# Kernel optimization log

Hardware: AMD Instinct MI355X
Metric: run time of the kernel (lower is better)

## Reference

```python
import jax, jax.numpy as jnp
import numpy as np

B, T, F, H, O = 256, 1024, 128, 512, 64
BN_EPS = 1e-5


def setup_inputs() -> dict:
    key = jax.random.key(0)
    ks = jax.random.split(key, 24)
    p = lambda k, shape: 0.02 * jax.random.normal(k, shape, dtype=jnp.float32)
    inp = {
        "x": jax.random.normal(ks[0], (B, T, F), dtype=jnp.float32),
        "delta": jax.random.uniform(ks[1], (B, T, F), dtype=jnp.float32),
        "m": (jax.random.uniform(ks[2], (B, T, F)) > 0.5).astype(jnp.float32),
        "x_forward": jax.random.normal(ks[3], (B, T, F), dtype=jnp.float32),
        # packed-sequence style: descending number of active rows per timestep
        "batch_sizes": jnp.sort(jax.random.randint(ks[4], (T,), 1, B + 1))[::-1].astype(jnp.int32),
        "W_r": p(ks[5], (F, H)), "U_r": p(ks[6], (H, H)), "V_r": p(ks[7], (F, H)), "b_r": jnp.zeros((H,), jnp.float32),
        "W_z": p(ks[8], (F, H)), "U_z": p(ks[9], (H, H)), "V_z": p(ks[10], (F, H)), "b_z": jnp.zeros((H,), jnp.float32),
        "W": p(ks[11], (F, H)), "U": p(ks[12], (H, H)), "V": p(ks[13], (F, H)), "b": jnp.zeros((H,), jnp.float32),
        "W_gamma_x": p(ks[14], (F,)), "b_gamma_x": jnp.zeros((F,), jnp.float32),
        "W_gamma_h": p(ks[15], (F, H)), "b_gamma_h": jnp.zeros((H,), jnp.float32),
        "dec_W": p(ks[16], (H, O)), "dec_b": jnp.zeros((O,), jnp.float32),
        "bn_w": jnp.ones((H,), jnp.float32), "bn_b": jnp.zeros((H,), jnp.float32),
    }
    return inp


def reference(x, delta, m, x_forward, batch_sizes,
              W_r, U_r, V_r, b_r, W_z, U_z, V_z, b_z, W, U, V, b,
              W_gamma_x, b_gamma_x, W_gamma_h, b_gamma_h,
              dec_W, dec_b, bn_w, bn_b):
    # input decay gamma_x: [B,T,F]; hidden decay gamma_h: [B,T,H]
    gamma_x = jnp.exp(-jax.nn.relu(delta * W_gamma_x + b_gamma_x))
    gamma_h = jnp.exp(-jax.nn.relu(jnp.einsum("btf,fh->bth", m, W_gamma_h) + b_gamma_h))
    # impute observed (m==1) positions with decayed forward-fill (matches x[m.byte()] = x_replace[m.byte()])
    x_rep = gamma_x * x_forward + (1.0 - gamma_x) * 0.001
    x = jnp.where(m > 0.5, x_rep, x)

    # time-major for scan
    xT = jnp.transpose(x, (1, 0, 2))        # [T,B,F]
    mT = jnp.transpose(m, (1, 0, 2))        # [T,B,F]
    gT = jnp.transpose(gamma_h, (1, 0, 2))  # [T,B,H]
    row = jnp.arange(B)

    def step(h, inp):
        x_t, m_t, g_t, bs = inp
        mask = (row < bs)[:, None]          # active rows this step
        h_d = jnp.where(mask, g_t * h, h)   # decayed hidden (index_copy_ on [:bs])
        one_m = 1.0 - m_t
        z = jax.nn.sigmoid(x_t @ W_z + h_d @ U_z + one_m @ V_z + b_z)
        r = jax.nn.sigmoid(x_t @ W_r + h_d @ U_r + one_m @ V_r + b_r)
        h_tilde = jnp.tanh(x_t @ W + (h_d * r) @ U + one_m @ V + b)
        h_new = jnp.where(mask, (1.0 - z) * h_d + z * h_tilde, h_d)
        return h_new, None

    h0 = jnp.zeros((B, H), jnp.float32)
    h_t, _ = jax.lax.scan(step, h0, (xT, mT, gT, batch_sizes))

    # eval-mode BatchNorm1d (running_mean=0, running_var=1); batch_size>1 so BN applies
    h_bn = h_t * (bn_w / jnp.sqrt(1.0 + BN_EPS)) + bn_b
    output = jax.nn.log_softmax(h_bn @ dec_W + dec_b, axis=-1)
    return output, h_bn
```

## Files before the change

kernel.cpp:

```cpp
#include <hip/hip_runtime.h>
#include <hip/hip_bf16.h>

typedef __attribute__((ext_vector_type(8))) short bf16x8;
typedef __attribute__((ext_vector_type(4))) float f32x4;
typedef __attribute__((ext_vector_type(4))) float fvec4;
typedef __attribute__((ext_vector_type(4))) unsigned short u16x4;
typedef __attribute__((ext_vector_type(4))) int i32x4;
typedef __attribute__((ext_vector_type(2))) unsigned int u32x2;

#define DEVI __device__ __forceinline__

constexpr int BB = 256, TT = 1024, FF = 128, HH = 512, OO = 64;
constexpr int KK = 256;
constexpr int NN = 2048;

DEVI unsigned short f2bf(float x) {
  unsigned int u = __float_as_uint(x);
  u += 0x7FFFu + ((u >> 16) & 1u);
  return (unsigned short)(u >> 16);
}
DEVI float bf2f(unsigned short s) {
  return __uint_as_float(((unsigned int)s) << 16);
}

DEVI void gload16(const void* g, void* lds) {
  __builtin_amdgcn_global_load_lds(
      (const __attribute__((address_space(1))) void*)g,
      (__attribute__((address_space(3))) void*)lds, 16, 0, 0);
}

DEVI void barrier_lds() {
  asm volatile("s_waitcnt lgkmcnt(0)" ::: "memory");
  __builtin_amdgcn_s_barrier();
  __builtin_amdgcn_sched_barrier(0);
}

DEVI int hgIdx(int row, int c) { return row*1024 + (c ^ ((row & 7) << 3)); }

__global__ __launch_bounds__(256) void prep_scales_kernel(
    const float* __restrict__ U_z, const float* __restrict__ U_r,
    const float* __restrict__ Uh, float* __restrict__ uscale)
{
  int n = blockIdx.x * 256 + threadIdx.x;
  if (n >= 1536) return;
  const float* src = (n < 512) ? U_z : (n < 1024) ? U_r : Uh;
  int col = n & 511;
  float s = 0.f;
  for (int k = 0; k < HH; ++k) s = fmaxf(s, fabsf(src[k*HH + col]));
  uscale[n] = fmaxf(s, 1e-30f);
}

__global__ __launch_bounds__(256) void prep_kernel(
    const float* __restrict__ W_z, const float* __restrict__ V_z, const float* __restrict__ b_z,
    const float* __restrict__ W_r, const float* __restrict__ V_r, const float* __restrict__ b_r,
    const float* __restrict__ Wh,  const float* __restrict__ Vh,  const float* __restrict__ bh,
    const float* __restrict__ Wgh, const float* __restrict__ bgh,
    const float* __restrict__ U_z, const float* __restrict__ U_r, const float* __restrict__ Uh,
    const float* __restrict__ uscale,
    unsigned short* __restrict__ BwT, float* __restrict__ bias,
    unsigned int* __restrict__ UzrN, int* __restrict__ UhQ)
{
  int idx = blockIdx.x * 256 + threadIdx.x;
  if (idx < 524288) {
    int n = idx >> 8, k = idx & 255;
    float v;
    if (n < 512)       { int h = n;        v = (k < 128) ? W_z[k*HH + h] : -V_z[(k-128)*HH + h]; }
    else if (n < 1024) { int h = n - 512;  v = (k < 128) ? W_r[k*HH + h] : -V_r[(k-128)*HH + h]; }
    else if (n < 1536) { int h = n - 1024; v = (k < 128) ? Wh [k*HH + h] : -Vh [(k-128)*HH + h]; }
    else               { int h = n - 1536; v = (k < 128) ? 0.f : Wgh[(k-128)*HH + h]; }
    BwT[n*256 + k] = f2bf(v);
    return;
  }
  idx -= 524288;
  if (idx < 2048) {
    int n = idx; float v;
    if (n < 512)       { float s = b_z[n];      for (int f = 0; f < FF; ++f) s += V_z[f*HH + n];        v = s; }
    else if (n < 1024) { int h = n-512;  float s = b_r[h]; for (int f = 0; f < FF; ++f) s += V_r[f*HH + h]; v = s; }
    else if (n < 1536) { int h = n-1024; float s = bh[h];  for (int f = 0; f < FF; ++f) s += Vh[f*HH + h];  v = s; }
    else               { v = bgh[n-1536]; }
    bias[n] = v;
    return;
  }
  idx -= 2048;
  if (idx < 65536) {
    int c  = idx & 1;
    int l  = (idx >> 1) & 63;
    int i  = (idx >> 7) & 3;
    int wv = (idx >> 9) & 7;
    int u  = idx >> 12;
    int kt = u >> 1, half = u & 1;
    int col = (wv*4 + i)*16 + (l & 15);
    const float* src = half ? U_r : U_z;
    float sc = 7.f / uscale[half*512 + col];
    unsigned int word = 0;
#pragma unroll
    for (int p = 0; p < 8; ++p) {
      int j = c*8 + (p & 1)*4 + (p >> 1);
      int k = kt*64 + (l >> 4)*16 + j;
      float q = fminf(fmaxf(rintf(src[k*HH + col] * sc), -7.f), 7.f);
      unsigned int uq = (unsigned int)((int)q + 8);
      word |= (uq & 0xF) << (4*p);
    }
    UzrN[idx] = word;
    return;
  }
  idx -= 65536;
  if (idx < 65536) {
    int j0 = (idx & 3) * 4;
    int l  = (idx >> 2) & 63;
    int nt = (idx >> 8) & 31;
    int kt = idx >> 13;
    int col = nt*16 + (l & 15);
    float sc = 127.f / uscale[1024 + col];
    int word = 0;
#pragma unroll
    for (int b = 0; b < 4; ++b) {
      int k = kt*64 + (l >> 4)*16 + j0 + b;
      float q = fminf(fmaxf(rintf(Uh[k*HH + col] * sc), -127.f), 127.f);
      word |= ((int)q & 0xFF) << (8*b);
    }
    UhQ[idx] = word;
  }
}

__global__ __launch_bounds__(256) void build_A_kernel(
    const float* __restrict__ x, const float* __restrict__ delta,
    const float* __restrict__ mm, const float* __restrict__ xf,
    const float* __restrict__ Wgx, const float* __restrict__ bgx,
    const int* __restrict__ bs, unsigned short* __restrict__ A,
    int t0, int TC)
{
  int blk = blockIdx.x;
  int row8 = blk * 8;
  int b0  = row8 / TC;
  int tl0 = row8 % TC;
  if (b0 >= bs[t0 + tl0]) return;
  int tid = threadIdx.x;
  int rl = row8 + (tid >> 5);
  int tc = tl0 + (tid >> 5);
  long gi = ((long)b0*TT + t0 + tc) * 32 + (tid & 31);
  int f0 = (tid & 31) * 4;
  fvec4 xv = ((const fvec4*)x)[gi];
  fvec4 dv = ((const fvec4*)delta)[gi];
  fvec4 mv = ((const fvec4*)mm)[gi];
  fvec4 fv = ((const fvec4*)xf)[gi];
  unsigned short ox[4], om[4];
#pragma unroll
  for (int j = 0; j < 4; ++j) {
    float g  = __expf(-fmaxf(dv[j]*Wgx[f0+j] + bgx[f0+j], 0.f));
    float xr = g*fv[j] + (1.f - g)*0.001f;
    float xi = (mv[j] > 0.5f) ? xr : xv[j];
    ox[j] = f2bf(xi); om[j] = f2bf(mv[j]);
  }
  *(u16x4*)(A + (long)rl*KK + f0)       = (u16x4){ox[0], ox[1], ox[2], ox[3]};
  *(u16x4*)(A + (long)rl*KK + 128 + f0) = (u16x4){om[0], om[1], om[2], om[3]};
}

__global__ __launch_bounds__(256) void gemm1_kernel(
    const unsigned short* __restrict__ A, const unsigned short* __restrict__ BwT,
    const float* __restrict__ bias, const int* __restrict__ bs,
    unsigned short* __restrict__ PRE, int t0, int TC)
{
  int blk = blockIdx.x;
  int nt = blk & 15;
  int mt = blk >> 4;
  {
    int m0 = mt * 128;
    int b_ = m0 / TC;
    int bcheck = (TC >= 128) ? bs[t0 + (m0 % TC)] : bs[t0];
    if (b_ >= bcheck) return;
  }
  int tid = threadIdx.x;
  int w = tid >> 6, l = tid & 63;
  int wm = w >> 1, wn = w & 1;
  int lr = l & 15, lg = l >> 4;
  int m_base = mt*128 + wm*64;
  int n_base = nt*128 + wn*64;
  const unsigned short* Aptr = A   + (long)(m_base + lr)*KK + lg*8;
  const unsigned short* Bptr = BwT + (long)(n_base + lr)*KK + lg*8;
  f32x4 acc[4][4];
#pragma unroll
  for (int i = 0; i < 4; ++i)
#pragma unroll
    for (int j = 0; j < 4; ++j) acc[i][j] = (f32x4){0.f, 0.f, 0.f, 0.f};

#pragma unroll
  for (int kt = 0; kt < 8; ++kt) {
    bf16x8 af[4], bfr[4];
#pragma unroll
    for (int i = 0; i < 4; ++i) af[i]  = *(const bf16x8*)(Aptr + (long)i*16*KK + kt*32);
#pragma unroll
    for (int i = 0; i < 4; ++i) bfr[i] = *(const bf16x8*)(Bptr + (long)i*16*KK + kt*32);
#pragma unroll
    for (int ms = 0; ms < 4; ++ms)
#pragma unroll
      for (int ns = 0; ns < 4; ++ns)
        acc[ms][ns] = __builtin_amdgcn_mfma_f32_16x16x32_bf16(af[ms], bfr[ns], acc[ms][ns], 0, 0, 0);
  }
#pragma unroll
  for (int ms = 0; ms < 4; ++ms) {
    int gm0 = m_base + ms*16 + lg*4;
#pragma unroll
    for (int ns = 0; ns < 4; ++ns) {
      int gn = n_base + ns*16 + lr;
      float bv = bias[gn];
      bool is_gamma = (gn >= 1536);
#pragma unroll
      for (int q = 0; q < 4; ++q) {
        float v = acc[ms][ns][q] + bv;
        if (is_gamma) v = __expf(-fmaxf(v, 0.f));
        PRE[(long)(gm0 + q)*NN + gn] = f2bf(v);
      }
    }
  }
}

__global__ __launch_bounds__(512, 2) void scan_kernel(
    const unsigned short* __restrict__ PRE,
    const unsigned int* __restrict__ UzrN,
    const signed char* __restrict__ UhQ,
    const float* __restrict__ uscale,
    const int* __restrict__ bs,
    float* __restrict__ h_st,
    float* __restrict__ sbuf,
    int t0, int TC)
{
  __shared__ __align__(16) signed char Ubuf[8][2][4096];
  __shared__ __align__(16) i32x4 hd_l[8*64];
  __shared__ __align__(16) unsigned short slabHG[16*1024];
  __shared__ float hm[16][524];
  __shared__ int hsumW[8][16];
  __shared__ float wmax[8];

  const int tid = threadIdx.x;
  const int r0 = blockIdx.x * 16;
  if (t0 > 0 && bs[t0] <= r0) return;

  const int w = tid >> 6, l = tid & 63, lr = l & 15, lg = l >> 4;
  const size_t rowStr = (size_t)TC * NN;

  signed char* slot0 = &Ubuf[w][0][0];
  signed char* slot1 = &Ubuf[w][1][0];

  auto STAGEB = [&](int u) {
    const signed char* src = UhQ + ((size_t)((u*32 + w*4)*64) + l)*16;
    signed char* dst = (u & 1) ? slot1 : slot0;
#pragma unroll
    for (int i = 0; i < 4; ++i) gload16(src + (size_t)i*1024, dst + i*1024);
  };
  auto STAGEHG = [&](const unsigned short* PREn) {
#pragma unroll
    for (int j = 0; j < 4; ++j) {
      int idx = w*4 + j;
      int row = idx >> 1;
      int phys = (idx & 1)*512 + l*8;
      int logi = phys ^ ((row & 7) << 3);
      const unsigned short* src = PREn + (size_t)row*rowStr + 1024 + logi;
      gload16(src, &slabHG[idx*512]);
    }
  };
  auto LOADZR = [&](int u, u32x2* d) {
#pragma unroll
    for (int i = 0; i < 4; ++i)
      d[i] = ((const u32x2*)UzrN)[((u*8 + w)*4 + i)*64 + l];
  };

  float zdq[4], rdq[4], hdq[4];
#pragma unroll
  for (int i = 0; i < 4; ++i) {
    int c = (w*4 + i)*16 + lr;
    zdq[i] = uscale[c]        * (1.f/889.f);
    rdq[i] = uscale[512 + c]  * (1.f/889.f);
    hdq[i] = uscale[1024 + c] * (1.f/16129.f);
  }
  if (tid < 8) wmax[tid] = (t0 == 0) ? 1e-20f : sbuf[blockIdx.x];

  if (t0 == 0) {
    for (int i = tid; i < 16*512; i += 512) hm[i>>9][i&511] = 0.f;
  } else {
    for (int i = tid; i < 16*512; i += 512)
      hm[i>>9][i&511] = h_st[(size_t)(r0 + (i>>9))*HH + (i&511)];
  }
  asm volatile("s_waitcnt vmcnt(0)" ::: "memory");
  __builtin_amdgcn_sched_barrier(0);

  STAGEHG(PRE + (size_t)r0*TC*NN);
  STAGEB(0); STAGEB(1);

  for (int tc = 0; tc < TC; ++tc) {
    const int bsv = bs[t0 + tc];
    if (bsv <= r0) break;
    const int na = min(16, bsv - r0);
    const unsigned short* PREstep = PRE + ((size_t)r0*TC + tc)*NN;
    const unsigned short* PREnext = PREstep + NN;

    barrier_lds();
    asm volatile("s_waitcnt vmcnt(8)" ::: "memory");
    __builtin_amdgcn_sched_barrier(0);

    float s = wmax[0];
#pragma unroll
    for (int i = 1; i < 8; ++i) s = fmaxf(s, wmax[i]);
    const float qs = 127.f / s;

    unsigned short pzr[2][4][4];
#pragma unroll
    for (int i = 0; i < 4; ++i)
#pragma unroll
      for (int q = 0; q < 4; ++q) {
        int row = lg*4 + q, col = (w*4 + i)*16 + lr;
        const unsigned short* pb = PREstep + (size_t)row*rowStr + col;
        pzr[0][i][q] = pb[0];
        pzr[1][i][q] = pb[512];
      }

    u32x2 inW0[4], inW1[4];
    LOADZR(0, inW0);
    LOADZR(1, inW1);

    {
      const int k0 = w*64 + lg*16;
      const bool act = lr < na;
      bf16x8 g0 = *(const bf16x8*)&slabHG[hgIdx(lr, 512 + k0)];
      bf16x8 g1 = *(const bf16x8*)&slabHG[hgIdx(lr, 512 + k0 + 8)];
      i32x4 qw;
      int psum = 0;
#pragma unroll
      for (int d = 0; d < 4; ++d) {
        int word = 0;
#pragma unroll
        for (int b = 0; b < 4; ++b) {
          int j = d*4 + b;
          float h  = hm[lr][k0 + j];
          float gv = bf2f((unsigned short)(j < 8 ? g0[j] : g1[j-8]));
          float hd = act ? gv*h : h;
          float q  = fminf(fmaxf(rintf(hd*qs), -127.f), 127.f);
          int qi = (int)q;
          psum += qi;
          word |= (qi & 0xFF) << (8*b);
        }
        qw[d] = word;
      }
      hd_l[w*64 + l] = qw;
      psum += __shfl_xor(psum, 16);
      psum += __shfl_xor(psum, 32);
      if (lg == 0) hsumW[w][lr] = psum;
    }

    float phv[4][4], ggv[4][4];
#pragma unroll
    for (int i = 0; i < 4; ++i)
#pragma unroll
      for (int q = 0; q < 4; ++q) {
        int row = lg*4 + q, col = (w*4 + i)*16 + lr;
        phv[i][q] = bf2f(slabHG[hgIdx(row, col)]);
        ggv[i][q] = bf2f(slabHG[hgIdx(row, 512 + col)]);
      }
    barrier_lds();

    i32x4 acc[8];
#pragma unroll
    for (int i = 0; i < 8; ++i) acc[i] = (i32x4){0, 0, 0, 0};
    i32x4 af;
#pragma unroll
    for (int u = 0; u < 16; ++u) {
      if (!(u & 1)) af = hd_l[(u>>1)*64 + l];
      u32x2* inw = (u & 1) ? inW1 : inW0;
      __builtin_amdgcn_s_setprio(1);
#pragma unroll
      for (int i = 0; i < 4; ++i) {
        unsigned int W0 = inw[i][0], W1 = inw[i][1];
        i32x4 bfr;
        bfr[0] = (int)(W0 & 0x0F0F0F0Fu);
        bfr[1] = (int)((W0 >> 4) & 0x0F0F0F0Fu);
        bfr[2] = (int)(W1 & 0x0F0F0F0Fu);
        bfr[3] = (int)((W1 >> 4) & 0x0F0F0F0Fu);
        acc[(u&1)*4 + i] = __builtin_amdgcn_mfma_i32_16x16x64_i8(af, bfr, acc[(u&1)*4 + i], 0, 0, 0);
      }
      __builtin_amdgcn_s_setprio(0);
      if (u < 14) LOADZR(u + 2, (u & 1) ? inW1 : inW0);
    }

    int rsum[4];
#pragma unroll
    for (int q = 0; q < 4; ++q) {
      int row = lg*4 + q, t = 0;
#pragma unroll
      for (int w2 = 0; w2 < 8; ++w2) t += hsumW[w2][row];
      rsum[q] = t * 8;
    }
    float zreg[4][4];
#pragma unroll
    for (int i = 0; i < 4; ++i)
#pragma unroll
      for (int q = 0; q < 4; ++q) {
        int row = lg*4 + q, col = (w*4 + i)*16 + lr;
        float az = bf2f(pzr[0][i][q]) + (float)(acc[i][q]   - rsum[q]) * zdq[i] * s;
        float ar = bf2f(pzr[1][i][q]) + (float)(acc[4+i][q] - rsum[q]) * rdq[i] * s;
        zreg[i][q] = 1.f/(1.f + __expf(-az));
        slabHG[hgIdx(row, col)] = f2bf(1.f/(1.f + __expf(-ar)));
      }
    barrier_lds();

    {
      const int k0 = w*64 + lg*16;
      bf16x8 r0v = *(const bf16x8*)&slabHG[hgIdx(lr, k0)];
      bf16x8 r1v = *(const bf16x8*)&slabHG[hgIdx(lr, k0 + 8)];
      i32x4 qw = hd_l[w*64 + l], nw;
#pragma unroll
      for (int d = 0; d < 4; ++d) {
        int word = qw[d], out = 0;
#pragma unroll
        for (int b = 0; b < 4; ++b) {
          int j = d*4 + b;
          int hq = (int)(signed char)((word >> (8*b)) & 0xFF);
          float rv = bf2f((unsigned short)(j < 8 ? r0v[j] : r1v[j-8]));
          float q = fminf(fmaxf(rintf((float)hq * rv), -127.f), 127.f);
          out |= ((int)q & 0xFF) << (8*b);
        }
        nw[d] = out;
      }
      hd_l[w*64 + l] = nw;
    }
    barrier_lds();

    i32x4 accB[4];
#pragma unroll
    for (int i = 0; i < 4; ++i) accB[i] = (i32x4){0, 0, 0, 0};
#pragma unroll
    for (int u = 0; u < 8; ++u) {
      asm volatile("s_waitcnt vmcnt(4)" ::: "memory");
      __builtin_amdgcn_sched_barrier(0);
      const signed char* buf = (u & 1) ? slot1 : slot0;
      i32x4 af2 = hd_l[u*64 + l];
      __builtin_amdgcn_s_setprio(1);
#pragma unroll
      for (int i = 0; i < 4; ++i) {
        i32x4 bfr = ((const i32x4*)buf)[i*64 + l];
        accB[i] = __builtin_amdgcn_mfma_i32_16x16x64_i8(af2, bfr, accB[i], 0, 0, 0);
      }
      __builtin_amdgcn_s_setprio(0);
      __builtin_amdgcn_sched_barrier(0);
      if (u < 6)       STAGEB(u + 2);
      else if (u == 6) STAGEHG(PREnext);
      else             STAGEB(0);
    }
    STAGEB(1);

    float mloc = 0.f;
#pragma unroll
    for (int i = 0; i < 4; ++i)
#pragma unroll
      for (int q = 0; q < 4; ++q) {
        int row = lg*4 + q, col = (w*4 + i)*16 + lr;
        float hval;
        if (row < na) {
          float ah = phv[i][q] + (float)accB[i][q] * hdq[i] * s;
          float e  = __expf(2.f*ah);
          float th = 1.f - 2.f/(e + 1.f);
          float hd = ggv[i][q] * hm[row][col];
          hval = hd + zreg[i][q]*(th - hd);
          hm[row][col] = hval;
        } else {
          hval = hm[row][col];
        }
        mloc = fmaxf(mloc, fabsf(hval));
      }
#pragma unroll
    for (int off = 32; off > 0; off >>= 1) mloc = fmaxf(mloc, __shfl_xor(mloc, off));
    if (l == 0) wmax[w] = fmaxf(mloc, 1e-20f);
  }

  asm volatile("s_waitcnt vmcnt(0)" ::: "memory");
  barrier_lds();
  for (int i = tid; i < 16*512; i += 512)
    h_st[(size_t)(r0 + (i>>9))*HH + (i&511)] = hm[i>>9][i&511];
  if (tid == 0) {
    float s = wmax[0];
#pragma unroll
    for (int i = 1; i < 8; ++i) s = fmaxf(s, wmax[i]);
    sbuf[blockIdx.x] = s;
  }
}

__global__ __launch_bounds__(64) void head_kernel(
    const float* __restrict__ h_state, const float* __restrict__ decW,
    const float* __restrict__ decb, const float* __restrict__ bnw,
    const float* __restrict__ bnb, float* __restrict__ out)
{
  int b = blockIdx.x, o = threadIdx.x;
  __shared__ float hbn[HH];
  const float s = rsqrtf(1.f + 1e-5f);
  for (int j = o; j < HH; j += 64)
    hbn[j] = h_state[(long)b*HH + j] * (bnw[j] * s) + bnb[j];
  __syncthreads();
  float acc = decb[o];
  for (int j = 0; j < HH; ++j) acc += hbn[j] * decW[j*OO + o];
  float mx = acc;
#pragma unroll
  for (int off = 32; off > 0; off >>= 1) mx = fmaxf(mx, __shfl_xor(mx, off));
  float ex = __expf(acc - mx);
  float sum = ex;
#pragma unroll
  for (int off = 32; off > 0; off >>= 1) sum += __shfl_xor(sum, off);
  out[(long)b*OO + o] = acc - mx - __logf(sum);
  for (int j = o; j < HH; j += 64)
    out[(long)BB*OO + (long)b*HH + j] = hbn[j];
}

extern "C" void kernel_launch(void* const* d_in, const int* in_sizes, int n_in,
                              void* d_out, int out_size, void* d_ws, size_t ws_size,
                              hipStream_t stream) {
  const float* x     = (const float*)d_in[0];
  const float* delta = (const float*)d_in[1];
  const float* mm    = (const float*)d_in[2];
  const float* xf    = (const float*)d_in[3];
  const int*   bs    = (const int*)  d_in[4];
  const float* W_r   = (const float*)d_in[5];
  const float* U_r   = (const float*)d_in[6];
  const float* V_r   = (const float*)d_in[7];
  const float* b_r   = (const float*)d_in[8];
  const float* W_z   = (const float*)d_in[9];
  const float* U_z   = (const float*)d_in[10];
  const float* V_z   = (const float*)d_in[11];
  const float* b_z   = (const float*)d_in[12];
  const float* W     = (const float*)d_in[13];
  const float* U     = (const float*)d_in[14];
  const float* V     = (const float*)d_in[15];
  const float* b     = (const float*)d_in[16];
  const float* Wgx   = (const float*)d_in[17];
  const float* bgx   = (const float*)d_in[18];
  const float* Wgh   = (const float*)d_in[19];
  const float* bgh   = (const float*)d_in[20];
  const float* decW  = (const float*)d_in[21];
  const float* decb  = (const float*)d_in[22];
  const float* bnw   = (const float*)d_in[23];
  const float* bnb   = (const float*)d_in[24];

  auto rnd = [](size_t v) { return (v + 255) & ~(size_t)255; };
  const size_t fixed_bytes = rnd((size_t)2048*256*2) + rnd(2048*4)
                           + rnd((size_t)256*1024) + rnd((size_t)256*1024)
                           + rnd(1536*4) + rnd(64)
                           + rnd((size_t)BB*HH*4);
  int TC = 0;
  const int cands[5] = {128, 64, 32, 16, 8};
  for (int i = 0; i < 5; ++i) {
    size_t need = fixed_bytes + rnd((size_t)BB*cands[i]*KK*2) + rnd((size_t)BB*cands[i]*NN*2);
    if (need <= ws_size) { TC = cands[i]; break; }
  }
  if (TC == 0) return;

  char* p = (char*)d_ws;
  auto alloc = [&](size_t bytes) { char* r = p; p += (bytes + 255) & ~(size_t)255; return r; };
  unsigned short* A_chunk = (unsigned short*)alloc((size_t)BB * TC * KK * 2);
  unsigned short* PREc    = (unsigned short*)alloc((size_t)BB * TC * NN * 2);
  unsigned short* BwT     = (unsigned short*)alloc((size_t)2048 * 256 * 2);
  float*          bias    = (float*)alloc(2048 * 4);
  unsigned int*   UzrN    = (unsigned int*)alloc((size_t)256 * 1024);
  int*            UhQ     = (int*)alloc((size_t)256 * 1024);
  float*          uscale  = (float*)alloc(1536 * 4);
  float*          sbuf    = (float*)alloc(64);
  float*          h_st    = (float*)alloc((size_t)BB * HH * 4);

  prep_scales_kernel<<<6, 256, 0, stream>>>(U_z, U_r, U, uscale);
  prep_kernel<<<2568, 256, 0, stream>>>(W_z, V_z, b_z, W_r, V_r, b_r, W, V, b,
                                        Wgh, bgh, U_z, U_r, U, uscale,
                                        BwT, bias, UzrN, UhQ);
  const int nch = TT / TC;
  for (int c = 0; c < nch; ++c) {
    int t0 = c * TC;
    build_A_kernel<<<BB*TC/8, 256, 0, stream>>>(x, delta, mm, xf, Wgx, bgx, bs,
                                                A_chunk, t0, TC);
    gemm1_kernel<<<(BB*TC/128)*16, 256, 0, stream>>>(A_chunk, BwT, bias, bs,
                                                     PREc, t0, TC);
    scan_kernel<<<16, 512, 0, stream>>>(PREc, UzrN, (const signed char*)UhQ,
                                        uscale, bs, h_st, sbuf, t0, TC);
  }
  head_kernel<<<256, 64, 0, stream>>>(h_st, decW, decb, bnw, bnb, (float*)d_out);
}
```

Baseline: 20.83 ms.

## Quantize U_h recurrent weights to int4 and deepen the staging pipeline

The candidate-state recurrent weight U_h is now stored as offset-4-bit nibbles instead of int8, which halves its bytes streamed per timestep. The nibbles are unpacked to int8 with masks before the i8 MFMA, and the +8 offset is removed with a per-row sum of the activations. The LDS staging for U_h grows from two to four slots, and the U_z/U_r register prefetch grows to four stages, with the wait counts adjusted to match. The trade is a coarser quantization of U_h, which costs accuracy, plus extra unpack ALU work and more registers.

```diff
diff --git a/kernel.cpp b/kernel.cpp
--- a/kernel.cpp
+++ b/kernel.cpp
@@ -58,7 +58,7 @@
     const float* __restrict__ U_z, const float* __restrict__ U_r, const float* __restrict__ Uh,
     const float* __restrict__ uscale,
     unsigned short* __restrict__ BwT, float* __restrict__ bias,
-    unsigned int* __restrict__ UzrN, int* __restrict__ UhQ)
+    unsigned int* __restrict__ UzrN, unsigned int* __restrict__ UhN)
 {
   int idx = blockIdx.x * 256 + threadIdx.x;
   if (idx < 524288) {
@@ -105,21 +105,24 @@
     return;
   }
   idx -= 65536;
-  if (idx < 65536) {
-    int j0 = (idx & 3) * 4;
-    int l  = (idx >> 2) & 63;
-    int nt = (idx >> 8) & 31;
-    int kt = idx >> 13;
-    int col = nt*16 + (l & 15);
-    float sc = 127.f / uscale[1024 + col];
-    int word = 0;
-#pragma unroll
-    for (int b = 0; b < 4; ++b) {
-      int k = kt*64 + (l >> 4)*16 + j0 + b;
-      float q = fminf(fmaxf(rintf(Uh[k*HH + col] * sc), -127.f), 127.f);
-      word |= ((int)q & 0xFF) << (8*b);
-    }
-    UhQ[idx] = word;
+  if (idx < 32768) {
+    int c  = idx & 1;
+    int l  = (idx >> 1) & 63;
+    int i  = (idx >> 7) & 3;
+    int wv = (idx >> 9) & 7;
+    int u  = idx >> 12;
+    int col = (wv*4 + i)*16 + (l & 15);
+    float sc = 7.f / uscale[1024 + col];
+    unsigned int word = 0;
+#pragma unroll
+    for (int p = 0; p < 8; ++p) {
+      int j = c*8 + (p & 1)*4 + (p >> 1);
+      int k = u*64 + (l >> 4)*16 + j;
+      float q = fminf(fmaxf(rintf(Uh[k*HH + col] * sc), -7.f), 7.f);
+      unsigned int uq = (unsigned int)((int)q + 8);
+      word |= (uq & 0xF) << (4*p);
+    }
+    UhN[idx] = word;
   }
 }
 
@@ -218,18 +221,19 @@
 __global__ __launch_bounds__(512, 2) void scan_kernel(
     const unsigned short* __restrict__ PRE,
     const unsigned int* __restrict__ UzrN,
-    const signed char* __restrict__ UhQ,
+    const unsigned int* __restrict__ UhN,
     const float* __restrict__ uscale,
     const int* __restrict__ bs,
     float* __restrict__ h_st,
     float* __restrict__ sbuf,
     int t0, int TC)
 {
-  __shared__ __align__(16) signed char Ubuf[8][2][4096];
+  __shared__ __align__(16) char Ubuf[8][4][2048];
   __shared__ __align__(16) i32x4 hd_l[8*64];
   __shared__ __align__(16) unsigned short slabHG[16*1024];
   __shared__ float hm[16][524];
   __shared__ int hsumW[8][16];
+  __shared__ int hsumW2[8][16];
   __shared__ float wmax[8];
 
   const int tid = threadIdx.x;
@@ -239,14 +243,11 @@
   const int w = tid >> 6, l = tid & 63, lr = l & 15, lg = l >> 4;
   const size_t rowStr = (size_t)TC * NN;
 
-  signed char* slot0 = &Ubuf[w][0][0];
-  signed char* slot1 = &Ubuf[w][1][0];
-
   auto STAGEB = [&](int u) {
-    const signed char* src = UhQ + ((size_t)((u*32 + w*4)*64) + l)*16;
-    signed char* dst = (u & 1) ? slot1 : slot0;
-#pragma unroll
-    for (int i = 0; i < 4; ++i) gload16(src + (size_t)i*1024, dst + i*1024);
+    const char* src = (const char*)UhN + ((size_t)(u*8 + w))*2048 + (size_t)l*16;
+    char* dst = &Ubuf[w][u & 3][0];
+    gload16(src, dst);
+    gload16(src + 1024, dst + 1024);
   };
   auto STAGEHG = [&](const unsigned short* PREn) {
 #pragma unroll
@@ -271,7 +272,7 @@
     int c = (w*4 + i)*16 + lr;
     zdq[i] = uscale[c]        * (1.f/889.f);
     rdq[i] = uscale[512 + c]  * (1.f/889.f);
-    hdq[i] = uscale[1024 + c] * (1.f/16129.f);
+    hdq[i] = uscale[1024 + c] * (1.f/889.f);
   }
   if (tid < 8) wmax[tid] = (t0 == 0) ? 1e-20f : sbuf[blockIdx.x];
 
@@ -295,7 +296,7 @@
     const unsigned short* PREnext = PREstep + NN;
 
     barrier_lds();
-    asm volatile("s_waitcnt vmcnt(8)" ::: "memory");
+    asm volatile("s_waitcnt vmcnt(4)" ::: "memory");
     __builtin_amdgcn_sched_barrier(0);
 
     float s = wmax[0];
@@ -314,16 +315,16 @@
         pzr[1][i][q] = pb[512];
       }
 
-    u32x2 inW0[4], inW1[4];
-    LOADZR(0, inW0);
-    LOADZR(1, inW1);
-
+    u32x2 inW[4][4];
+    LOADZR(0, inW[0]); LOADZR(1, inW[1]);
+    LOADZR(2, inW[2]); LOADZR(3, inW[3]);
+
+    i32x4 qwReg;
     {
       const int k0 = w*64 + lg*16;
       const bool act = lr < na;
       bf16x8 g0 = *(const bf16x8*)&slabHG[hgIdx(lr, 512 + k0)];
       bf16x8 g1 = *(const bf16x8*)&slabHG[hgIdx(lr, 512 + k0 + 8)];
-      i32x4 qw;
       int psum = 0;
 #pragma unroll
       for (int d = 0; d < 4; ++d) {
@@ -339,9 +340,9 @@
           psum += qi;
           word |= (qi & 0xFF) << (8*b);
         }
-        qw[d] = word;
-      }
-      hd_l[w*64 + l] = qw;
+        qwReg[d] = word;
+      }
+      hd_l[w*64 + l] = qwReg;
       psum += __shfl_xor(psum, 16);
       psum += __shfl_xor(psum, 32);
       if (lg == 0) hsumW[w][lr] = psum;
@@ -365,7 +366,7 @@
 #pragma unroll
     for (int u = 0; u < 16; ++u) {
       if (!(u & 1)) af = hd_l[(u>>1)*64 + l];
-      u32x2* inw = (u & 1) ? inW1 : inW0;
+      u32x2* inw = inW[u & 3];
       __builtin_amdgcn_s_setprio(1);
 #pragma unroll
       for (int i = 0; i < 4; ++i) {
@@ -378,8 +379,9 @@
         acc[(u&1)*4 + i] = __builtin_amdgcn_mfma_i32_16x16x64_i8(af, bfr, acc[(u&1)*4 + i], 0, 0, 0);
       }
       __builtin_amdgcn_s_setprio(0);
-      if (u < 14) LOADZR(u + 2, (u & 1) ? inW1 : inW0);
-    }
+      if (u < 12) LOADZR(u + 4, inW[u & 3]);
+    }
+    STAGEB(2); STAGEB(3);
 
     int rsum[4];
 #pragma unroll
@@ -406,21 +408,27 @@
       const int k0 = w*64 + lg*16;
       bf16x8 r0v = *(const bf16x8*)&slabHG[hgIdx(lr, k0)];
       bf16x8 r1v = *(const bf16x8*)&slabHG[hgIdx(lr, k0 + 8)];
-      i32x4 qw = hd_l[w*64 + l], nw;
+      i32x4 nw;
+      int psum2 = 0;
 #pragma unroll
       for (int d = 0; d < 4; ++d) {
-        int word = qw[d], out = 0;
+        int word = qwReg[d], out = 0;
 #pragma unroll
         for (int b = 0; b < 4; ++b) {
           int j = d*4 + b;
           int hq = (int)(signed char)((word >> (8*b)) & 0xFF);
           float rv = bf2f((unsigned short)(j < 8 ? r0v[j] : r1v[j-8]));
           float q = fminf(fmaxf(rintf((float)hq * rv), -127.f), 127.f);
-          out |= ((int)q & 0xFF) << (8*b);
+          int qi = (int)q;
+          psum2 += qi;
+          out |= (qi & 0xFF) << (8*b);
         }
         nw[d] = out;
       }
       hd_l[w*64 + l] = nw;
+      psum2 += __shfl_xor(psum2, 16);
+      psum2 += __shfl_xor(psum2, 32);
+      if (lg == 0) hsumW2[w][lr] = psum2;
     }
     barrier_lds();
 
@@ -429,24 +437,39 @@
     for (int i = 0; i < 4; ++i) accB[i] = (i32x4){0, 0, 0, 0};
 #pragma unroll
     for (int u = 0; u < 8; ++u) {
-      asm volatile("s_waitcnt vmcnt(4)" ::: "memory");
+      if (u < 5) { asm volatile("s_waitcnt vmcnt(6)" ::: "memory"); }
+      else       { asm volatile("s_waitcnt vmcnt(8)" ::: "memory"); }
       __builtin_amdgcn_sched_barrier(0);
-      const signed char* buf = (u & 1) ? slot1 : slot0;
+      const char* buf = &Ubuf[w][u & 3][0];
       i32x4 af2 = hd_l[u*64 + l];
       __builtin_amdgcn_s_setprio(1);
 #pragma unroll
       for (int i = 0; i < 4; ++i) {
-        i32x4 bfr = ((const i32x4*)buf)[i*64 + l];
+        u32x2 Wv = *(const u32x2*)&buf[(i*64 + l)*8];
+        unsigned int W0 = Wv[0], W1 = Wv[1];
+        i32x4 bfr;
+        bfr[0] = (int)(W0 & 0x0F0F0F0Fu);
+        bfr[1] = (int)((W0 >> 4) & 0x0F0F0F0Fu);
+        bfr[2] = (int)(W1 & 0x0F0F0F0Fu);
+        bfr[3] = (int)((W1 >> 4) & 0x0F0F0F0Fu);
         accB[i] = __builtin_amdgcn_mfma_i32_16x16x64_i8(af2, bfr, accB[i], 0, 0, 0);
       }
       __builtin_amdgcn_s_setprio(0);
       __builtin_amdgcn_sched_barrier(0);
-      if (u < 6)       STAGEB(u + 2);
-      else if (u == 6) STAGEHG(PREnext);
-      else             STAGEB(0);
-    }
-    STAGEB(1);
-
+      if (u < 4)       STAGEB(u + 4);
+      else if (u == 4) STAGEHG(PREnext);
+      else if (u == 5) STAGEB(0);
+      else if (u == 6) STAGEB(1);
+    }
+
+    int rsum2[4];
+#pragma unroll
+    for (int q = 0; q < 4; ++q) {
+      int row = lg*4 + q, t = 0;
+#pragma unroll
+      for (int w2 = 0; w2 < 8; ++w2) t += hsumW2[w2][row];
+      rsum2[q] = t * 8;
+    }
     float mloc = 0.f;
 #pragma unroll
     for (int i = 0; i < 4; ++i)
@@ -455,7 +478,7 @@
         int row = lg*4 + q, col = (w*4 + i)*16 + lr;
         float hval;
         if (row < na) {
-          float ah = phv[i][q] + (float)accB[i][q] * hdq[i] * s;
+          float ah = phv[i][q] + (float)(accB[i][q] - rsum2[q]) * hdq[i] * s;
           float e  = __expf(2.f*ah);
           float th = 1.f - 2.f/(e + 1.f);
           float hd = ggv[i][q] * hm[row][col];
@@ -539,7 +562,7 @@
 
   auto rnd = [](size_t v) { return (v + 255) & ~(size_t)255; };
   const size_t fixed_bytes = rnd((size_t)2048*256*2) + rnd(2048*4)
-                           + rnd((size_t)256*1024) + rnd((size_t)256*1024)
+                           + rnd((size_t)256*1024) + rnd((size_t)128*1024)
                            + rnd(1536*4) + rnd(64)
                            + rnd((size_t)BB*HH*4);
   int TC = 0;
@@ -557,15 +580,15 @@
   unsigned short* BwT     = (unsigned short*)alloc((size_t)2048 * 256 * 2);
   float*          bias    = (float*)alloc(2048 * 4);
   unsigned int*   UzrN    = (unsigned int*)alloc((size_t)256 * 1024);
-  int*            UhQ     = (int*)alloc((size_t)256 * 1024);
+  unsigned int*   UhN     = (unsigned int*)alloc((size_t)128 * 1024);
   float*          uscale  = (float*)alloc(1536 * 4);
   float*          sbuf    = (float*)alloc(64);
   float*          h_st    = (float*)alloc((size_t)BB * HH * 4);
 
   prep_scales_kernel<<<6, 256, 0, stream>>>(U_z, U_r, U, uscale);
-  prep_kernel<<<2568, 256, 0, stream>>>(W_z, V_z, b_z, W_r, V_r, b_r, W, V, b,
+  prep_kernel<<<2440, 256, 0, stream>>>(W_z, V_z, b_z, W_r, V_r, b_r, W, V, b,
                                         Wgh, bgh, U_z, U_r, U, uscale,
-                                        BwT, bias, UzrN, UhQ);
+                                        BwT, bias, UzrN, UhN);
   const int nch = TT / TC;
   for (int c = 0; c < nch; ++c) {
     int t0 = c * TC;
@@ -573,8 +596,8 @@
                                                 A_chunk, t0, TC);
     gemm1_kernel<<<(BB*TC/128)*16, 256, 0, stream>>>(A_chunk, BwT, bias, bs,
                                                      PREc, t0, TC);
-    scan_kernel<<<16, 512, 0, stream>>>(PREc, UzrN, (const signed char*)UhQ,
-                                        uscale, bs, h_st, sbuf, t0, TC);
+    scan_kernel<<<16, 512, 0, stream>>>(PREc, UzrN, UhN, uscale, bs,
+                                        h_st, sbuf, t0, TC);
   }
   head_kernel<<<256, 64, 0, stream>>>(h_st, decW, decb, bnw, bnb, (float*)d_out);
 }
```

Measured after the change: 19.58 ms. 6.0% less time.
